# Optimization experiments

Measured on AMD Instinct MI355X. Metric: run time of the kernel, lower is better.

Reference implementation:

```python
import jax, jax.numpy as jnp
import numpy as np

N = 10000
E = 80000


def gat_layer(x, src, dst, W, a_src, a_dst, b):
    # x: [N, Fin], W: [Fin, Fout]
    xw = x @ W                              # [N, Fout]
    al_src = xw @ a_src                     # [N]
    al_dst = xw @ a_dst                     # [N]
    e = jax.nn.leaky_relu(al_src[src] + al_dst[dst], 0.2)  # [E+N]
    m = jax.lax.stop_gradient(jax.ops.segment_max(e, dst, num_segments=N))
    ex = jnp.exp(e - m[dst])
    denom = jax.ops.segment_sum(ex, dst, num_segments=N)
    alpha = ex / (denom[dst] + 1e-16)       # PyG softmax eps
    out = jax.ops.segment_sum(alpha[:, None] * xw[src], dst, num_segments=N)
    return out + b


def setup_inputs() -> dict:
    key = jax.random.key(0)
    ks = jax.random.split(key, 12)
    x = jax.random.normal(ks[0], (N, 256), dtype=jnp.float32)
    edge_index = jax.random.randint(ks[1], (2, E), 0, N, dtype=jnp.int64)
    def glorot(k, fi, fo):
        return jax.random.normal(k, (fi, fo), jnp.float32) * jnp.sqrt(2.0 / (fi + fo))
    W1 = glorot(ks[2], 256, 2048)
    W2 = glorot(ks[3], 2048, 2048)
    W3 = glorot(ks[4], 2048, 1024)
    a1s = jax.random.normal(ks[5], (2048,), jnp.float32) * 0.05
    a1d = jax.random.normal(ks[6], (2048,), jnp.float32) * 0.05
    a2s = jax.random.normal(ks[7], (2048,), jnp.float32) * 0.05
    a2d = jax.random.normal(ks[8], (2048,), jnp.float32) * 0.05
    a3s = jax.random.normal(ks[9], (1024,), jnp.float32) * 0.05
    a3d = jax.random.normal(ks[10], (1024,), jnp.float32) * 0.05
    b1 = jnp.zeros((2048,), jnp.float32)
    b2 = jnp.zeros((2048,), jnp.float32)
    b3 = jnp.zeros((1024,), jnp.float32)
    return {"x": x, "edge_index": edge_index, "W1": W1, "W2": W2, "W3": W3,
            "a1s": a1s, "a1d": a1d, "a2s": a2s, "a2d": a2d, "a3s": a3s, "a3d": a3d,
            "b1": b1, "b2": b2, "b3": b3}


def reference(x, edge_index, W1, W2, W3, a1s, a1d, a2s, a2d, a3s, a3d, b1, b2, b3):
    # add self loops (PyG GATConv default add_self_loops=True)
    loop = jnp.arange(N, dtype=edge_index.dtype)
    src = jnp.concatenate([edge_index[0], loop])
    dst = jnp.concatenate([edge_index[1], loop])
    h = jax.nn.relu(gat_layer(x, src, dst, W1, a1s, a1d, b1))
    h = jax.nn.relu(gat_layer(h, src, dst, W2, a2s, a2d, b2))
    h = jax.nn.relu(gat_layer(h, src, dst, W3, a3s, a3d, b3))
    # F.normalize(dim=1), eps=1e-12
    norm = jnp.linalg.norm(h, axis=1, keepdims=True)
    return h / jnp.maximum(norm, 1e-12)
```

## Files before the change

kernel.cpp:

```cpp
#include <hip/hip_runtime.h>
#include <hip/hip_bf16.h>
#include <math.h>


typedef __attribute__((ext_vector_type(8))) short short8;
typedef __attribute__((ext_vector_type(4))) float f32x4;

#define GLOAD_LDS16(g, l)                                            \
  __builtin_amdgcn_global_load_lds(                                  \
      (const __attribute__((address_space(1))) void*)(g),            \
      (__attribute__((address_space(3))) void*)(l), 16, 0, 0)

__device__ __forceinline__ float bf16_to_f32(ushort u) {
  return __uint_as_float(((unsigned int)u) << 16);
}

__device__ __forceinline__ float block_reduce_sum_bcast(float v) {
#pragma unroll
  for (int off = 32; off > 0; off >>= 1) v += __shfl_down(v, off, 64);
  __shared__ float tmp[4];
  __shared__ float res;
  int lane = threadIdx.x & 63, w = threadIdx.x >> 6;
  if (lane == 0) tmp[w] = v;
  __syncthreads();
  if (threadIdx.x == 0) res = tmp[0] + tmp[1] + tmp[2] + tmp[3];
  __syncthreads();
  float out = res;
  __syncthreads();
  return out;
}

__device__ __forceinline__ float block_reduce_max_bcast(float v) {
#pragma unroll
  for (int off = 32; off > 0; off >>= 1) v = fmaxf(v, __shfl_down(v, off, 64));
  __shared__ float tmpm[4];
  __shared__ float resm;
  int lane = threadIdx.x & 63, w = threadIdx.x >> 6;
  if (lane == 0) tmpm[w] = v;
  __syncthreads();
  if (threadIdx.x == 0) resm = fmaxf(fmaxf(tmpm[0], tmpm[1]), fmaxf(tmpm[2], tmpm[3]));
  __syncthreads();
  float out = resm;
  __syncthreads();
  return out;
}

__global__ void detect_kernel(const int* __restrict__ ei32, int* __restrict__ flag) {
  __shared__ int cnt;
  if (threadIdx.x == 0) cnt = 0;
  __syncthreads();
  int zeros = 0;
  for (int i = threadIdx.x; i < 1024; i += 256) {
    if (ei32[2 * i + 1] == 0) zeros++;
  }
  atomicAdd(&cnt, zeros);
  __syncthreads();
  if (threadIdx.x == 0) *flag = (cnt > 900) ? 1 : 0;
}

__global__ void convert_kernel(const void* __restrict__ ei, const int* __restrict__ flag,
                               int E, int* __restrict__ src, int* __restrict__ dst) {
  int i = blockIdx.x * blockDim.x + threadIdx.x;
  if (i >= E) return;
  if (*flag) {
    const long long* p = (const long long*)ei;
    src[i] = (int)p[i];
    dst[i] = (int)p[E + i];
  } else {
    const int* p = (const int*)ei;
    src[i] = p[i];
    dst[i] = p[E + i];
  }
}

__global__ __launch_bounds__(256) void convert_f32_bf16(const float* __restrict__ in,
                                                        __hip_bfloat16* __restrict__ out,
                                                        int n) {
  int i = blockIdx.x * blockDim.x + threadIdx.x;
  if (i < n) out[i] = __float2bfloat16(in[i]);
}

__global__ __launch_bounds__(256) void transpose_w(const float* __restrict__ W,
                                                   __hip_bfloat16* __restrict__ Wt,
                                                   int K, int Nout) {
  __shared__ float t[32][33];
  int tx = threadIdx.x & 31, ty = threadIdx.x >> 5;
  int n0 = blockIdx.x * 32, k0 = blockIdx.y * 32;
#pragma unroll
  for (int i = 0; i < 4; ++i) {
    int k = k0 + ty + i * 8;
    t[ty + i * 8][tx] = W[(size_t)k * Nout + n0 + tx];
  }
  __syncthreads();
#pragma unroll
  for (int i = 0; i < 4; ++i) {
    int n = n0 + ty + i * 8;
    Wt[(size_t)n * K + k0 + tx] = __float2bfloat16(t[tx][ty + i * 8]);
  }
}

template <bool BF16OUT>
__global__ __launch_bounds__(256) void gemm_bf16(const ushort* __restrict__ A,
                                                 const ushort* __restrict__ Bt,
                                                 void* __restrict__ C,
                                                 int M, int K, int Nout) {
  __shared__ ushort As[128 * 32];
  __shared__ ushort Bs[128 * 32];
  int tid = threadIdx.x;
  int lane = tid & 63, w = tid >> 6;
  int wr = (w >> 1) * 64, wc = (w & 1) * 64;
  int l15 = lane & 15, lhi = lane >> 4;
  int row0 = blockIdx.y * 128, col0 = blockIdx.x * 128;

  int srow = w * 32 + (lane >> 2);
  int scol = (lane & 3) * 8;
  ushort* la0 = &As[(w * 32) * 32];
  ushort* la1 = &As[(w * 32 + 16) * 32];
  ushort* lb0 = &Bs[(w * 32) * 32];
  ushort* lb1 = &Bs[(w * 32 + 16) * 32];
  int ar0 = min(row0 + srow, M - 1);
  int ar1 = min(row0 + srow + 16, M - 1);
  const ushort* gb0 = Bt + (size_t)(col0 + srow) * K + scol;
  const ushort* gb1 = Bt + (size_t)(col0 + srow + 16) * K + scol;
  const ushort* ga0 = A + (size_t)ar0 * K + scol;
  const ushort* ga1 = A + (size_t)ar1 * K + scol;

  f32x4 acc[4][4] = {};

  for (int k0 = 0; k0 < K; k0 += 32) {
    GLOAD_LDS16(ga0 + k0, la0);
    GLOAD_LDS16(ga1 + k0, la1);
    GLOAD_LDS16(gb0 + k0, lb0);
    GLOAD_LDS16(gb1 + k0, lb1);
    __syncthreads();
    short8 af[4], bfr[4];
#pragma unroll
    for (int m = 0; m < 4; ++m)
      af[m] = *(const short8*)(&As[(wr + m * 16 + l15) * 32 + lhi * 8]);
#pragma unroll
    for (int n = 0; n < 4; ++n)
      bfr[n] = *(const short8*)(&Bs[(wc + n * 16 + l15) * 32 + lhi * 8]);
#pragma unroll
    for (int m = 0; m < 4; ++m)
#pragma unroll
      for (int n = 0; n < 4; ++n)
        acc[m][n] = __builtin_amdgcn_mfma_f32_16x16x32_bf16(af[m], bfr[n], acc[m][n], 0, 0, 0);
    __syncthreads();
  }

#pragma unroll
  for (int m = 0; m < 4; ++m) {
#pragma unroll
    for (int v = 0; v < 4; ++v) {
      int r = row0 + wr + m * 16 + lhi * 4 + v;
      if (r < M) {
#pragma unroll
        for (int n = 0; n < 4; ++n) {
          size_t idx = (size_t)r * Nout + col0 + wc + n * 16 + l15;
          if (BF16OUT)
            ((__hip_bfloat16*)C)[idx] = __float2bfloat16(acc[m][n][v]);
          else
            ((float*)C)[idx] = acc[m][n][v];
        }
      }
    }
  }
}

template <bool BF16IN>
__global__ __launch_bounds__(256) void compute_al(const void* __restrict__ xw,
                                                  const float* __restrict__ a_s,
                                                  const float* __restrict__ a_d,
                                                  float* __restrict__ als,
                                                  float* __restrict__ ald, int F) {
  int n = blockIdx.x;
  float s1 = 0.f, s2 = 0.f;
  if (BF16IN) {
    const ushort* row = (const ushort*)xw + (size_t)n * F;
    int base = threadIdx.x * 8;
    short8 v = *(const short8*)(row + base);
#pragma unroll
    for (int j = 0; j < 8; ++j) {
      float f = bf16_to_f32((ushort)v[j]);
      s1 += f * a_s[base + j];
      s2 += f * a_d[base + j];
    }
  } else {
    const float* row = (const float*)xw + (size_t)n * F;
    for (int f = threadIdx.x; f < F; f += 256) {
      float v = row[f];
      s1 += v * a_s[f];
      s2 += v * a_d[f];
    }
  }
  float r1 = block_reduce_sum_bcast(s1);
  float r2 = block_reduce_sum_bcast(s2);
  if (threadIdx.x == 0) {
    als[n] = r1;
    ald[n] = r2;
  }
}

__global__ void count_kernel(const int* __restrict__ dst, int* __restrict__ counts, int E) {
  int i = blockIdx.x * blockDim.x + threadIdx.x;
  if (i < E) atomicAdd(&counts[dst[i]], 1);
}

__global__ __launch_bounds__(1024) void scan_kernel(const int* __restrict__ counts,
                                                    int* __restrict__ rowptr,
                                                    int* __restrict__ cursor, int Nn) {
  __shared__ int part[1024];
  int tid = threadIdx.x;
  int chunk = (Nn + 1023) / 1024;
  int base = tid * chunk;
  int s = 0;
  for (int i = 0; i < chunk; ++i) {
    int idx = base + i;
    if (idx < Nn) s += counts[idx];
  }
  part[tid] = s;
  __syncthreads();
  for (int off = 1; off < 1024; off <<= 1) {
    int v = 0;
    if (tid >= off) v = part[tid - off];
    __syncthreads();
    if (tid >= off) part[tid] += v;
    __syncthreads();
  }
  int run = (tid == 0) ? 0 : part[tid - 1];
  for (int i = 0; i < chunk; ++i) {
    int idx = base + i;
    if (idx < Nn) {
      rowptr[idx] = run;
      cursor[idx] = run;
      run += counts[idx];
    }
  }
  if (tid == 1023) rowptr[Nn] = part[1023];
}

__global__ void fill_kernel(const int* __restrict__ src, const int* __restrict__ dst,
                            int* __restrict__ cursor, int* __restrict__ eidx, int E) {
  int i = blockIdx.x * blockDim.x + threadIdx.x;
  if (i < E) {
    int pos = atomicAdd(&cursor[dst[i]], 1);
    eidx[pos] = src[i];
  }
}

template <int FPT, bool BF16IN, bool BF16OUT>
__global__ __launch_bounds__(256) void aggregate(const void* __restrict__ xw,
                                                 const float* __restrict__ als,
                                                 const float* __restrict__ ald,
                                                 const int* __restrict__ rowptr,
                                                 const int* __restrict__ eidx,
                                                 const float* __restrict__ bias,
                                                 void* __restrict__ out, int F) {
  int n = blockIdx.x;
  int tid = threadIdx.x;
  int beg = rowptr[n], end = rowptr[n + 1];
  int deg = end - beg;
  float aldn = ald[n];

  float lm = -INFINITY;
  for (int j = tid; j < deg; j += 256) {
    int s = eidx[beg + j];
    float e = als[s] + aldn;
    e = (e > 0.f) ? e : 0.2f * e;
    lm = fmaxf(lm, e);
  }
  if (tid == 0) {
    float e = als[n] + aldn;
    e = (e > 0.f) ? e : 0.2f * e;
    lm = fmaxf(lm, e);
  }
  float m = block_reduce_max_bcast(lm);

  float ls = 0.f;
  for (int j = tid; j < deg; j += 256) {
    int s = eidx[beg + j];
    float e = als[s] + aldn;
    e = (e > 0.f) ? e : 0.2f * e;
    ls += expf(e - m);
  }
  if (tid == 0) {
    float e = als[n] + aldn;
    e = (e > 0.f) ? e : 0.2f * e;
    ls += expf(e - m);
  }
  float denom = block_reduce_sum_bcast(ls) + 1e-16f;
  float inv_denom = 1.f / denom;

  float acc[FPT];
#pragma unroll
  for (int i = 0; i < FPT; ++i) acc[i] = 0.f;

  __shared__ float alpha_sh[256];
  __shared__ int src_sh[256];
  int total = deg + 1;
  for (int c0 = 0; c0 < total; c0 += 256) {
    int j = c0 + tid;
    if (j < total) {
      int s = (j < deg) ? eidx[beg + j] : n;
      float e = als[s] + aldn;
      e = (e > 0.f) ? e : 0.2f * e;
      alpha_sh[tid] = expf(e - m) * inv_denom;
      src_sh[tid] = s;
    }
    __syncthreads();
    int cn = min(256, total - c0);
    for (int jj = 0; jj < cn; ++jj) {
      float al = alpha_sh[jj];
      if (BF16IN) {
        const ushort* row = (const ushort*)xw + (size_t)src_sh[jj] * F;
#pragma unroll
        for (int i = 0; i < FPT / 2; ++i) {
          unsigned int u = *(const unsigned int*)(row + tid * 2 + i * 512);
          acc[2 * i]     += al * __uint_as_float((u & 0xffffu) << 16);
          acc[2 * i + 1] += al * __uint_as_float(u & 0xffff0000u);
        }
      } else {
        const float* row = (const float*)xw + (size_t)src_sh[jj] * F;
#pragma unroll
        for (int i = 0; i < FPT; ++i) acc[i] += al * row[tid + i * 256];
      }
    }
    __syncthreads();
  }

#pragma unroll
  for (int i = 0; i < FPT; ++i) {
    int col = BF16IN ? (tid * 2 + (i >> 1) * 512 + (i & 1)) : (tid + i * 256);
    float v = fmaxf(acc[i] + bias[col], 0.f);
    size_t idx = (size_t)n * F + col;
    if (BF16OUT)
      ((__hip_bfloat16*)out)[idx] = __float2bfloat16(v);
    else
      ((float*)out)[idx] = v;
  }
}

__global__ __launch_bounds__(256) void normalize_kernel(const float* __restrict__ h,
                                                        float* __restrict__ out,
                                                        int F) {
  int n = blockIdx.x;
  const float* row = h + (size_t)n * F;
  float ss = 0.f;
  for (int f = threadIdx.x; f < F; f += 256) {
    float v = row[f];
    ss += v * v;
  }
  float tot = block_reduce_sum_bcast(ss);
  float inv = 1.f / fmaxf(sqrtf(tot), 1e-12f);
  for (int f = threadIdx.x; f < F; f += 256) {
    out[(size_t)n * F + f] = row[f] * inv;
  }
}

extern "C" void kernel_launch(void* const* d_in, const int* in_sizes, int n_in,
                              void* d_out, int out_size, void* d_ws, size_t ws_size,
                              hipStream_t stream) {
  const float* x   = (const float*)d_in[0];
  const void*  ei  = d_in[1];
  const float* W1  = (const float*)d_in[2];
  const float* W2  = (const float*)d_in[3];
  const float* W3  = (const float*)d_in[4];
  const float* a1s = (const float*)d_in[5];
  const float* a1d = (const float*)d_in[6];
  const float* a2s = (const float*)d_in[7];
  const float* a2d = (const float*)d_in[8];
  const float* a3s = (const float*)d_in[9];
  const float* a3d = (const float*)d_in[10];
  const float* b1  = (const float*)d_in[11];
  const float* b2  = (const float*)d_in[12];
  const float* b3  = (const float*)d_in[13];

  const int N = in_sizes[0] / 256;
  const int E = in_sizes[1] / 2;

  char* ws = (char*)d_ws;
  size_t off = 0;
  auto alloc = [&](size_t bytes) -> void* {
    void* p = ws + off;
    off += (bytes + 255) & ~(size_t)255;
    return p;
  };
  ushort* xwb = (ushort*)alloc((size_t)N * 2048 * 2);
  ushort* hbf = (ushort*)alloc((size_t)N * 2048 * 2);
  float* bufA = (float*)alloc((size_t)N * 1024 * 4);
  __hip_bfloat16* xb  = (__hip_bfloat16*)alloc((size_t)N * 256 * 2);
  __hip_bfloat16* Wt1 = (__hip_bfloat16*)alloc((size_t)2048 * 256 * 2);
  __hip_bfloat16* Wt2 = (__hip_bfloat16*)alloc((size_t)2048 * 2048 * 2);
  __hip_bfloat16* Wt3 = (__hip_bfloat16*)alloc((size_t)1024 * 2048 * 2);
  float* als   = (float*)alloc((size_t)N * 4);
  float* ald   = (float*)alloc((size_t)N * 4);
  int* counts  = (int*)alloc((size_t)N * 4);
  int* rowptr  = (int*)alloc((size_t)(N + 1) * 4);
  int* cursor  = (int*)alloc((size_t)N * 4);
  int* eidx    = (int*)alloc((size_t)E * 4);
  int* src32   = (int*)alloc((size_t)E * 4);
  int* dst32   = (int*)alloc((size_t)E * 4);
  int* flag    = (int*)alloc(256);

  detect_kernel<<<1, 256, 0, stream>>>((const int*)ei, flag);
  convert_kernel<<<(E + 255) / 256, 256, 0, stream>>>(ei, flag, E, src32, dst32);
  hipMemsetAsync(counts, 0, (size_t)N * 4, stream);
  count_kernel<<<(E + 255) / 256, 256, 0, stream>>>(dst32, counts, E);
  scan_kernel<<<1, 1024, 0, stream>>>(counts, rowptr, cursor, N);
  fill_kernel<<<(E + 255) / 256, 256, 0, stream>>>(src32, dst32, cursor, eidx, E);

  convert_f32_bf16<<<(N * 256 + 255) / 256, 256, 0, stream>>>(x, xb, N * 256);
  transpose_w<<<dim3(2048 / 32, 256 / 32), 256, 0, stream>>>(W1, Wt1, 256, 2048);
  transpose_w<<<dim3(2048 / 32, 2048 / 32), 256, 0, stream>>>(W2, Wt2, 2048, 2048);
  transpose_w<<<dim3(1024 / 32, 2048 / 32), 256, 0, stream>>>(W3, Wt3, 2048, 1024);

  dim3 blk(256);
  int mb = (N + 127) / 128;

  gemm_bf16<true><<<dim3(2048 / 128, mb), blk, 0, stream>>>((const ushort*)xb, (const ushort*)Wt1, xwb, N, 256, 2048);
  compute_al<true><<<N, blk, 0, stream>>>(xwb, a1s, a1d, als, ald, 2048);
  aggregate<8, true, true><<<N, blk, 0, stream>>>(xwb, als, ald, rowptr, eidx, b1, hbf, 2048);

  gemm_bf16<true><<<dim3(2048 / 128, mb), blk, 0, stream>>>(hbf, (const ushort*)Wt2, xwb, N, 2048, 2048);
  compute_al<true><<<N, blk, 0, stream>>>(xwb, a2s, a2d, als, ald, 2048);
  aggregate<8, true, true><<<N, blk, 0, stream>>>(xwb, als, ald, rowptr, eidx, b2, hbf, 2048);

  gemm_bf16<false><<<dim3(1024 / 128, mb), blk, 0, stream>>>(hbf, (const ushort*)Wt3, bufA, N, 2048, 1024);
  compute_al<false><<<N, blk, 0, stream>>>(bufA, a3s, a3d, als, ald, 1024);
  float* hf32 = (float*)xwb;
  aggregate<4, false, false><<<N, blk, 0, stream>>>(bufA, als, ald, rowptr, eidx, b3, hf32, 1024);

  normalize_kernel<<<N, blk, 0, stream>>>(hf32, (float*)d_out, 1024);
}
```

Measured before the change: 477.3 us.

## Replace GEMM with 256x256 tile, double-buffered LDS pipeline and swizzled layout

```diff
diff --git a/kernel.cpp b/kernel.cpp
--- a/kernel.cpp
+++ b/kernel.cpp
@@ -100,71 +100,109 @@
 }
 
 template <bool BF16OUT>
-__global__ __launch_bounds__(256) void gemm_bf16(const ushort* __restrict__ A,
-                                                 const ushort* __restrict__ Bt,
-                                                 void* __restrict__ C,
-                                                 int M, int K, int Nout) {
-  __shared__ ushort As[128 * 32];
-  __shared__ ushort Bs[128 * 32];
-  int tid = threadIdx.x;
-  int lane = tid & 63, w = tid >> 6;
-  int wr = (w >> 1) * 64, wc = (w & 1) * 64;
-  int l15 = lane & 15, lhi = lane >> 4;
-  int row0 = blockIdx.y * 128, col0 = blockIdx.x * 128;
-
-  int srow = w * 32 + (lane >> 2);
-  int scol = (lane & 3) * 8;
-  ushort* la0 = &As[(w * 32) * 32];
-  ushort* la1 = &As[(w * 32 + 16) * 32];
-  ushort* lb0 = &Bs[(w * 32) * 32];
-  ushort* lb1 = &Bs[(w * 32 + 16) * 32];
-  int ar0 = min(row0 + srow, M - 1);
-  int ar1 = min(row0 + srow + 16, M - 1);
-  const ushort* gb0 = Bt + (size_t)(col0 + srow) * K + scol;
-  const ushort* gb1 = Bt + (size_t)(col0 + srow + 16) * K + scol;
-  const ushort* ga0 = A + (size_t)ar0 * K + scol;
-  const ushort* ga1 = A + (size_t)ar1 * K + scol;
-
-  f32x4 acc[4][4] = {};
-
-  for (int k0 = 0; k0 < K; k0 += 32) {
-    GLOAD_LDS16(ga0 + k0, la0);
-    GLOAD_LDS16(ga1 + k0, la1);
-    GLOAD_LDS16(gb0 + k0, lb0);
-    GLOAD_LDS16(gb1 + k0, lb1);
-    __syncthreads();
-    short8 af[4], bfr[4];
-#pragma unroll
-    for (int m = 0; m < 4; ++m)
-      af[m] = *(const short8*)(&As[(wr + m * 16 + l15) * 32 + lhi * 8]);
-#pragma unroll
-    for (int n = 0; n < 4; ++n)
-      bfr[n] = *(const short8*)(&Bs[(wc + n * 16 + l15) * 32 + lhi * 8]);
-#pragma unroll
-    for (int m = 0; m < 4; ++m)
-#pragma unroll
-      for (int n = 0; n < 4; ++n)
-        acc[m][n] = __builtin_amdgcn_mfma_f32_16x16x32_bf16(af[m], bfr[n], acc[m][n], 0, 0, 0);
-    __syncthreads();
-  }
-
-#pragma unroll
-  for (int m = 0; m < 4; ++m) {
+__global__ __launch_bounds__(512, 2) void gemm256(const ushort* __restrict__ A,
+                                                  const ushort* __restrict__ Bt,
+                                                  void* __restrict__ C,
+                                                  int M, int K, int Nout) {
+  extern __shared__ ushort lds[];
+  const int tid = threadIdx.x;
+  const int l = tid & 63, w = tid >> 6;
+  const int wm = w >> 2, wn = w & 3;
+  const int l15 = l & 15, lhi = l >> 4;
+  const int row0 = blockIdx.y * 256, col0 = blockIdx.x * 256;
+  const int c8sw = (l & 3) ^ (((l >> 5) & 1) << 1);
+  const int lrow = l >> 2;
+  const int chsw = lhi ^ (((l15 >> 3) & 1) << 1);
+  const int rd_off = l15 * 32 + chsw * 8;
+
+  const ushort* ga[2][2];
+  const ushort* gb[2][2];
+  const int sA0 = wm * 8 + wn * 2;
+  const int sB0 = (wn >> 1) * 8 + (wm * 2 + (wn & 1)) * 2;
+#pragma unroll
+  for (int sc = 0; sc < 2; ++sc) {
+#pragma unroll
+    for (int j = 0; j < 2; ++j) {
+      int ar = min(row0 + (sA0 + j) * 16 + lrow, M - 1);
+      ga[sc][j] = A + (size_t)ar * K + sc * 32 + c8sw * 8;
+      gb[sc][j] = Bt + (size_t)(col0 + (sB0 + j) * 16 + lrow) * K + sc * 32 + c8sw * 8;
+    }
+  }
+
+#define STAGE_A(nb, kn, sc)                                                       \
+  do {                                                                            \
+    GLOAD_LDS16(ga[sc][0] + (kn), &lds[(nb)*32768 + ((sA0 + 0) * 2 + (sc)) * 512]); \
+    GLOAD_LDS16(ga[sc][1] + (kn), &lds[(nb)*32768 + ((sA0 + 1) * 2 + (sc)) * 512]); \
+  } while (0)
+#define STAGE_B(nb, kn, sc)                                                       \
+  do {                                                                            \
+    GLOAD_LDS16(gb[sc][0] + (kn), &lds[(nb)*32768 + 16384 + ((sB0 + 0) * 2 + (sc)) * 512]); \
+    GLOAD_LDS16(gb[sc][1] + (kn), &lds[(nb)*32768 + 16384 + ((sB0 + 1) * 2 + (sc)) * 512]); \
+  } while (0)
+
+  f32x4 acc[8][4] = {};
+
+#define PHASE(cur, mh, kk, STAGE_STMT)                                            \
+  do {                                                                            \
+    short8 af[4], bf[4];                                                          \
+    const ushort* Ab = &lds[(cur)*32768];                                         \
+    const ushort* Bb = &lds[(cur)*32768 + 16384];                                 \
+    _Pragma("unroll") for (int m = 0; m < 4; ++m)                                 \
+        af[m] = *(const short8*)(Ab + ((wm * 8 + (mh)*4 + m) * 2 + (kk)) * 512 + rd_off); \
+    _Pragma("unroll") for (int n = 0; n < 4; ++n)                                 \
+        bf[n] = *(const short8*)(Bb + ((wn * 4 + n) * 2 + (kk)) * 512 + rd_off);  \
+    STAGE_STMT;                                                                   \
+    asm volatile("s_waitcnt vmcnt(4)" ::: "memory");                              \
+    __builtin_amdgcn_s_barrier();                                                 \
+    __builtin_amdgcn_s_setprio(1);                                                \
+    _Pragma("unroll") for (int m = 0; m < 4; ++m)                                 \
+        _Pragma("unroll") for (int n = 0; n < 4; ++n)                             \
+            acc[(mh)*4 + m][n] = __builtin_amdgcn_mfma_f32_16x16x32_bf16(         \
+                af[m], bf[n], acc[(mh)*4 + m][n], 0, 0, 0);                       \
+    __builtin_amdgcn_s_setprio(0);                                                \
+    __builtin_amdgcn_s_barrier();                                                 \
+  } while (0)
+
+  STAGE_A(0, 0, 0);
+  STAGE_B(0, 0, 0);
+  STAGE_A(0, 0, 1);
+  STAGE_B(0, 0, 1);
+  asm volatile("s_waitcnt vmcnt(0)" ::: "memory");
+  __builtin_amdgcn_s_barrier();
+
+  const int nt = K >> 6;
+  int cur = 0;
+  for (int t = 0; t < nt; ++t) {
+    const int kn = (t + 1) << 6;
+    const bool pf = (t + 1) < nt;
+    const int nb = cur ^ 1;
+    PHASE(cur, 0, 0, if (pf) STAGE_A(nb, kn, 0));
+    PHASE(cur, 1, 0, if (pf) STAGE_B(nb, kn, 0));
+    PHASE(cur, 0, 1, if (pf) STAGE_A(nb, kn, 1));
+    PHASE(cur, 1, 1, if (pf) STAGE_B(nb, kn, 1));
+    cur ^= 1;
+  }
+
+#pragma unroll
+  for (int mi = 0; mi < 8; ++mi) {
 #pragma unroll
     for (int v = 0; v < 4; ++v) {
-      int r = row0 + wr + m * 16 + lhi * 4 + v;
+      int r = row0 + wm * 128 + mi * 16 + lhi * 4 + v;
       if (r < M) {
 #pragma unroll
         for (int n = 0; n < 4; ++n) {
-          size_t idx = (size_t)r * Nout + col0 + wc + n * 16 + l15;
+          size_t idx = (size_t)r * Nout + col0 + wn * 64 + n * 16 + l15;
           if (BF16OUT)
-            ((__hip_bfloat16*)C)[idx] = __float2bfloat16(acc[m][n][v]);
+            ((__hip_bfloat16*)C)[idx] = __float2bfloat16(acc[mi][n][v]);
           else
-            ((float*)C)[idx] = acc[m][n][v];
+            ((float*)C)[idx] = acc[mi][n][v];
         }
       }
     }
   }
+#undef PHASE
+#undef STAGE_A
+#undef STAGE_B
 }
 
 template <bool BF16IN>
@@ -402,6 +440,15 @@
   int* dst32   = (int*)alloc((size_t)E * 4);
   int* flag    = (int*)alloc(256);
 
+  static bool attr_done = false;
+  if (!attr_done) {
+    hipFuncSetAttribute((const void*)gemm256<true>,
+                        hipFuncAttributeMaxDynamicSharedMemorySize, 131072);
+    hipFuncSetAttribute((const void*)gemm256<false>,
+                        hipFuncAttributeMaxDynamicSharedMemorySize, 131072);
+    attr_done = true;
+  }
+
   detect_kernel<<<1, 256, 0, stream>>>((const int*)ei, flag);
   convert_kernel<<<(E + 255) / 256, 256, 0, stream>>>(ei, flag, E, src32, dst32);
   hipMemsetAsync(counts, 0, (size_t)N * 4, stream);
@@ -415,17 +462,18 @@
   transpose_w<<<dim3(1024 / 32, 2048 / 32), 256, 0, stream>>>(W3, Wt3, 2048, 1024);
 
   dim3 blk(256);
-  int mb = (N + 127) / 128;
-
-  gemm_bf16<true><<<dim3(2048 / 128, mb), blk, 0, stream>>>((const ushort*)xb, (const ushort*)Wt1, xwb, N, 256, 2048);
+  dim3 gblk(512);
+  int mb = (N + 255) / 256;
+
+  gemm256<true><<<dim3(2048 / 256, mb), gblk, 131072, stream>>>((const ushort*)xb, (const ushort*)Wt1, xwb, N, 256, 2048);
   compute_al<true><<<N, blk, 0, stream>>>(xwb, a1s, a1d, als, ald, 2048);
   aggregate<8, true, true><<<N, blk, 0, stream>>>(xwb, als, ald, rowptr, eidx, b1, hbf, 2048);
 
-  gemm_bf16<true><<<dim3(2048 / 128, mb), blk, 0, stream>>>(hbf, (const ushort*)Wt2, xwb, N, 2048, 2048);
+  gemm256<true><<<dim3(2048 / 256, mb), gblk, 131072, stream>>>(hbf, (const ushort*)Wt2, xwb, N, 2048, 2048);
   compute_al<true><<<N, blk, 0, stream>>>(xwb, a2s, a2d, als, ald, 2048);
   aggregate<8, true, true><<<N, blk, 0, stream>>>(xwb, als, ald, rowptr, eidx, b2, hbf, 2048);
 
-  gemm_bf16<false><<<dim3(1024 / 128, mb), blk, 0, stream>>>(hbf, (const ushort*)Wt3, bufA, N, 2048, 1024);
+  gemm256<false><<<dim3(1024 / 256, mb), gblk, 131072, stream>>>(hbf, (const ushort*)Wt3, bufA, N, 2048, 1024);
   compute_al<false><<<N, blk, 0, stream>>>(bufA, a3s, a3d, als, ald, 1024);
   float* hf32 = (float*)xwb;
   aggregate<4, false, false><<<N, blk, 0, stream>>>(bufA, als, ald, rowptr, eidx, b3, hf32, 1024);
```

New measurement: 474.6 us. About the same (-0.6%).
